# Kernel optimization log

Measured on AMD Instinct MI355X. Metric: run time of the kernel, lower is better.

The kernel has to match this reference:

```python
import jax, jax.numpy as jnp
import numpy as np

B, N, F, H = 2, 2048, 1024, 16
HD = F // H
SQRT_D = float(np.sqrt(F))  # note: module scales by sqrt(in_c), not sqrt(head_dim)


def setup_inputs() -> dict:
    key = jax.random.key(0)
    ks = jax.random.split(key, 9)
    s = 1.0 / np.sqrt(F)
    mk = lambda k: jax.random.uniform(k, (F, F), jnp.float32, -s, s)
    mb = lambda k: jax.random.uniform(k, (F,), jnp.float32, -s, s)
    return {
        "x": jax.random.normal(ks[0], (B, N, F), jnp.float32),
        "Wq": mk(ks[1]), "bq": mb(ks[2]),
        "Wk": mk(ks[3]), "bk": mb(ks[4]),
        "Wv": mk(ks[5]), "bv": mb(ks[6]),
        "Wo": mk(ks[7]), "bo": mb(ks[8]),
    }


def reference(x, Wq, bq, Wk, bk, Wv, bv, Wo, bo):
    b, n, f = x.shape
    # projections (torch Linear: x @ W.T + b); view to (b, n, h, hd)
    q = (x @ Wq.T + bq).reshape(b, n, H, HD)
    k = (x @ Wk.T + bk).reshape(b, n, H, HD)
    v = (x @ Wv.T + bv).reshape(b, n, H, HD)
    score = jnp.einsum('bihd,bjhd->bhij', q, k)
    attn = jax.nn.softmax(score / SQRT_D, axis=-1)
    o = jnp.einsum('bhij,bjhd->bihd', attn, v).reshape(b, n, f)
    return o @ Wo.T + bo
```

## Files before the change

### kernel.cpp

```cpp
#include <hip/hip_runtime.h>
#include <hip/hip_bf16.h>
#include <stdint.h>
#include <stddef.h>

typedef __bf16 bf16;
typedef __attribute__((ext_vector_type(8))) __bf16 bf16x8;
typedef __attribute__((ext_vector_type(4))) __bf16 bf16x4;
typedef __attribute__((ext_vector_type(4))) float f32x4;
typedef __attribute__((ext_vector_type(4))) short s4v;

#define MFMA16(a, b, c) __builtin_amdgcn_mfma_f32_16x16x32_bf16(a, b, c, 0, 0, 0)

__device__ __forceinline__ f32x4 mfma_k16(s4v a, s4v b, f32x4 c) {
#if __has_builtin(__builtin_amdgcn_mfma_f32_16x16x16bf16_1k)
    return __builtin_amdgcn_mfma_f32_16x16x16bf16_1k(a, b, c, 0, 0, 0);
#elif __has_builtin(__builtin_amdgcn_mfma_f32_16x16x16_bf16)
    return __builtin_amdgcn_mfma_f32_16x16x16_bf16(
        __builtin_bit_cast(bf16x4, a), __builtin_bit_cast(bf16x4, b), c, 0, 0, 0);
#else
    asm volatile("v_mfma_f32_16x16x16_bf16 %0, %1, %2, %0\n\ts_nop 7\n\ts_nop 7"
                 : "+v"(c) : "v"(a), "v"(b));
    return c;
#endif
}

#define BB 2
#define SEQ 2048
#define FDIM 1024
#define NH 16
#define HD 64
#define M_TOK 4096
#define N_QKV 3072

#define CSC 0.04508422f

__device__ __forceinline__ void gll16(const bf16* g, bf16* l) {
    __builtin_amdgcn_global_load_lds(
        (const __attribute__((address_space(1))) void*)g,
        (__attribute__((address_space(3))) void*)l, 16, 0, 0);
}

__device__ __forceinline__ bf16 pack_bf16(float f) {
    uint32_t u = __builtin_bit_cast(uint32_t, f);
    uint16_t h = (uint16_t)((u + 0x8000u) >> 16);
    return __builtin_bit_cast(bf16, h);
}

__global__ __launch_bounds__(256) void convert_k(
    const float* __restrict__ x,
    const float* __restrict__ Wq, const float* __restrict__ bq,
    const float* __restrict__ Wk, const float* __restrict__ bk,
    const float* __restrict__ Wv, const float* __restrict__ bv,
    const float* __restrict__ Wo,
    bf16* __restrict__ xb, bf16* __restrict__ Wcat, bf16* __restrict__ Wob,
    float* __restrict__ bcat)
{
    const int tid = blockIdx.x * blockDim.x + threadIdx.x;
    const int nt = gridDim.x * blockDim.x;
    const int NX4 = M_TOK * FDIM / 4;
    const int NW4 = FDIM * FDIM / 4;

    for (int i = tid; i < NX4; i += nt) {
        float4 v = ((const float4*)x)[i];
        bf16x4 o; o[0] = (bf16)v.x; o[1] = (bf16)v.y; o[2] = (bf16)v.z; o[3] = (bf16)v.w;
        ((bf16x4*)xb)[i] = o;
    }
    for (int i = tid; i < NW4; i += nt) {
        float4 v = ((const float4*)Wq)[i];
        bf16x4 o;
        o[0] = (bf16)(v.x * CSC); o[1] = (bf16)(v.y * CSC);
        o[2] = (bf16)(v.z * CSC); o[3] = (bf16)(v.w * CSC);
        ((bf16x4*)Wcat)[i] = o;
        v = ((const float4*)Wk)[i];
        o[0] = (bf16)v.x; o[1] = (bf16)v.y; o[2] = (bf16)v.z; o[3] = (bf16)v.w;
        ((bf16x4*)Wcat)[NW4 + i] = o;
        v = ((const float4*)Wv)[i];
        o[0] = (bf16)v.x; o[1] = (bf16)v.y; o[2] = (bf16)v.z; o[3] = (bf16)v.w;
        ((bf16x4*)Wcat)[2 * NW4 + i] = o;
        v = ((const float4*)Wo)[i];
        o[0] = (bf16)v.x; o[1] = (bf16)v.y; o[2] = (bf16)v.z; o[3] = (bf16)v.w;
        ((bf16x4*)Wob)[i] = o;
    }
    for (int i = tid; i < FDIM; i += nt) {
        bcat[i] = bq[i] * CSC;
        bcat[FDIM + i] = bk[i];
        bcat[2 * FDIM + i] = bv[i];
    }
}

__global__ __launch_bounds__(256) void gemm_bt(
    const bf16* __restrict__ A,
    const bf16* __restrict__ Bw,
    const float* __restrict__ bias,
    bf16* __restrict__ Cb,
    float* __restrict__ Cf,
    bf16* __restrict__ VtOut,
    int M, int N, int K)
{
    __shared__ __align__(16) bf16 As[2][128 * 32];
    __shared__ __align__(16) bf16 Bs[2][128 * 32];

    const int tid = threadIdx.x;
    const int lane = tid & 63;
    const int wave = tid >> 6;
    const int m0 = blockIdx.y * 128;
    const int n0 = blockIdx.x * 128;
    const int wm = (wave >> 1) * 64;
    const int wn = (wave & 1) * 64;
    const int lrow = lane & 15;
    const int lk8 = (lane >> 4) * 8;

    f32x4 acc[4][4] = {};

    const int srow = wave * 16 + (lane >> 2);
    const int scol = (lane & 3) * 8;
    const bf16* Ag = A + (size_t)(m0 + srow) * K + scol;
    const bf16* Bg = Bw + (size_t)(n0 + srow) * K + scol;
    const int wo = (wave * 16) * 32;

    gll16(Ag, &As[0][wo]);
    gll16(Ag + (size_t)64 * K, &As[0][wo + 2048]);
    gll16(Bg, &Bs[0][wo]);
    gll16(Bg + (size_t)64 * K, &Bs[0][wo + 2048]);

    for (int k0 = 0, it = 0; k0 < K; k0 += 32, ++it) {
        const int cur = it & 1;
        __syncthreads();

        if (k0 + 32 < K) {
            const int nxt = cur ^ 1;
            gll16(Ag + k0 + 32, &As[nxt][wo]);
            gll16(Ag + (size_t)64 * K + k0 + 32, &As[nxt][wo + 2048]);
            gll16(Bg + k0 + 32, &Bs[nxt][wo]);
            gll16(Bg + (size_t)64 * K + k0 + 32, &Bs[nxt][wo + 2048]);
        }

        bf16x8 af[4], bfr[4];
#pragma unroll
        for (int s = 0; s < 4; ++s) {
            af[s] = *(const bf16x8*)&As[cur][(wm + s * 16 + lrow) * 32 + lk8];
            bfr[s] = *(const bf16x8*)&Bs[cur][(wn + s * 16 + lrow) * 32 + lk8];
        }
#pragma unroll
        for (int i = 0; i < 4; ++i)
#pragma unroll
            for (int j = 0; j < 4; ++j)
                acc[i][j] = MFMA16(af[i], bfr[j], acc[i][j]);
    }

    const int r0 = (lane >> 4) * 4;
    if (VtOut && n0 >= 2048) {
        const int bql = (m0 >> 11);
#pragma unroll
        for (int i = 0; i < 4; ++i) {
#pragma unroll
            for (int j = 0; j < 4; ++j) {
                const int col = n0 + wn + j * 16 + lrow;
                const float bsv = bias[col];
                const int vh = col - 2048;
                const int row = m0 + wm + i * 16 + r0;
                const int jj = row & (SEQ - 1);
                bf16x4 vv;
#pragma unroll
                for (int r = 0; r < 4; ++r)
                    vv[r] = pack_bf16(acc[i][j][r] + bsv);
                *(bf16x4*)&VtOut[((size_t)bql * 16 * 64 + vh) * SEQ + jj] = vv;
            }
        }
        return;
    }
#pragma unroll
    for (int i = 0; i < 4; ++i) {
#pragma unroll
        for (int j = 0; j < 4; ++j) {
            const int col = n0 + wn + j * 16 + lrow;
            const float bsv = bias[col];
#pragma unroll
            for (int r = 0; r < 4; ++r) {
                const int row = m0 + wm + i * 16 + r0 + r;
                const float v = acc[i][j][r] + bsv;
                if (Cb) Cb[(size_t)row * N + col] = pack_bf16(v);
                else    Cf[(size_t)row * N + col] = v;
            }
        }
    }
}

__global__ __launch_bounds__(256) void attn_k(
    const bf16* __restrict__ QKV,
    const bf16* __restrict__ Vt,
    bf16* __restrict__ O)
{
    const int bh = blockIdx.y;
    const int b = bh >> 4;
    const int h = bh & 15;
    const int lane = threadIdx.x & 63;
    const int wave = threadIdx.x >> 6;
    const int lrow = lane & 15;
    const int quad = lane >> 4;
    const int lk8 = quad * 8;

    __shared__ __align__(16) bf16 Ks[2][2][64 * 32];
    __shared__ __align__(16) bf16 Vs[2][2][64 * 32];

    const size_t base = (size_t)b * SEQ * N_QKV;
    const bf16* Qp = QKV + base + h * HD;
    const bf16* Kp = QKV + base + FDIM + h * HD;
    const bf16* Vtp = Vt + (size_t)bh * HD * SEQ;

    const int qr0 = blockIdx.x * 128 + wave * 32;

    bf16x8 qf[2][2];
#pragma unroll
    for (int qt = 0; qt < 2; ++qt)
#pragma unroll
        for (int ks = 0; ks < 2; ++ks)
            qf[qt][ks] = *(const bf16x8*)(Qp + (size_t)(qr0 + qt * 16 + lrow) * N_QKV
                                          + ks * 32 + lk8);

    bf16x4 ones4;
#pragma unroll
    for (int e = 0; e < 4; ++e) ones4[e] = (bf16)1.0f;
    const s4v onesA = __builtin_bit_cast(s4v, ones4);

    f32x4 o[2][4] = {};
    f32x4 o4[2] = {};

    const int xsw = lrow & 3;
    const int qh = quad >> 1;
    const int ql = (quad & 1) * 4;
    int voff[2][4];
#pragma unroll
    for (int p = 0; p < 2; ++p)
#pragma unroll
        for (int df = 0; df < 4; ++df)
            voff[p][df] = (df * 16 + lrow) * 32 + (((2 * p + qh) ^ xsw) * 8) + ql;

    const int srow = wave * 16 + (lane >> 2);
    const int scol = (lane & 3) * 8;
    const int scolv = (((lane & 3) ^ (srow & 3)) * 8);
    const bf16* kg = Kp + (size_t)srow * N_QKV + scol;
    const bf16* vg = Vtp + (size_t)srow * SEQ + scolv;
    const int wo = (wave * 16) * 32;

    gll16(kg, &Ks[0][0][wo]);
    gll16(kg + 32, &Ks[0][1][wo]);
    gll16(vg, &Vs[0][0][wo]);
    gll16(vg + 32, &Vs[0][1][wo]);
    kg += (size_t)64 * N_QKV;
    vg += 64;

    for (int jt = 0; jt < SEQ / 64; ++jt) {
        const int cur = jt & 1;
        __syncthreads();

        if (jt + 1 < SEQ / 64) {
            gll16(kg, &Ks[cur ^ 1][0][wo]);
            gll16(kg + 32, &Ks[cur ^ 1][1][wo]);
            gll16(vg, &Vs[cur ^ 1][0][wo]);
            gll16(vg + 32, &Vs[cur ^ 1][1][wo]);
            kg += (size_t)64 * N_QKV;
            vg += 64;
        }

        f32x4 Sp[4][2];
#pragma unroll
        for (int jn = 0; jn < 4; ++jn)
#pragma unroll
            for (int qt = 0; qt < 2; ++qt) Sp[jn][qt] = (f32x4){};
#pragma unroll
        for (int ks = 0; ks < 2; ++ks) {
#pragma unroll
            for (int jn = 0; jn < 4; ++jn) {
                bf16x8 kb = *(const bf16x8*)&Ks[cur][ks][(jn * 16 + lrow) * 32 + lk8];
                Sp[jn][0] = MFMA16(kb, qf[0][ks], Sp[jn][0]);
                Sp[jn][1] = MFMA16(kb, qf[1][ks], Sp[jn][1]);
            }
        }

        s4v pB[4][2];
#pragma unroll
        for (int jn = 0; jn < 4; ++jn)
#pragma unroll
            for (int qt = 0; qt < 2; ++qt) {
                bf16x4 t;
#pragma unroll
                for (int r = 0; r < 4; ++r)
                    t[r] = pack_bf16(__builtin_amdgcn_exp2f(Sp[jn][qt][r]));
                pB[jn][qt] = __builtin_bit_cast(s4v, t);
            }

#pragma unroll
        for (int jn = 0; jn < 4; ++jn) {
            const bf16* vbase = &Vs[cur][jn >> 1][0];
            o4[0] = mfma_k16(onesA, pB[jn][0], o4[0]);
            o4[1] = mfma_k16(onesA, pB[jn][1], o4[1]);
#pragma unroll
            for (int df = 0; df < 4; ++df) {
                s4v vA = *(const s4v*)&vbase[voff[jn & 1][df]];
                o[0][df] = mfma_k16(vA, pB[jn][0], o[0][df]);
                o[1][df] = mfma_k16(vA, pB[jn][1], o[1][df]);
            }
        }
    }

#pragma unroll
    for (int qt = 0; qt < 2; ++qt) {
        const float inv = 1.0f / o4[qt][0];
        const int q = qr0 + qt * 16 + lrow;
#pragma unroll
        for (int df = 0; df < 4; ++df) {
            bf16x4 vv;
#pragma unroll
            for (int r = 0; r < 4; ++r)
                vv[r] = pack_bf16(o[qt][df][r] * inv);
            *(bf16x4*)&O[(size_t)(b * SEQ + q) * FDIM + h * HD + df * 16 + quad * 4] = vv;
        }
    }
}

extern "C" void kernel_launch(void* const* d_in, const int* in_sizes, int n_in,
                              void* d_out, int out_size, void* d_ws, size_t ws_size,
                              hipStream_t stream) {
    (void)in_sizes; (void)n_in; (void)out_size; (void)ws_size;
    const float* x  = (const float*)d_in[0];
    const float* Wq = (const float*)d_in[1];
    const float* bq = (const float*)d_in[2];
    const float* Wk = (const float*)d_in[3];
    const float* bk = (const float*)d_in[4];
    const float* Wv = (const float*)d_in[5];
    const float* bv = (const float*)d_in[6];
    const float* Wo = (const float*)d_in[7];
    const float* bo = (const float*)d_in[8];
    float* out = (float*)d_out;

    char* ws = (char*)d_ws;
    bf16* xb    = (bf16*)(ws);
    bf16* Wcat  = (bf16*)(ws + 8388608);
    bf16* Wob   = (bf16*)(ws + 14680064);
    float* bcat = (float*)(ws + 16777216);
    bf16* QKV   = (bf16*)(ws + 16789504);
    bf16* Vt    = (bf16*)(ws + 41955328);
    bf16* Ob    = xb;

    convert_k<<<dim3(1024), dim3(256), 0, stream>>>(x, Wq, bq, Wk, bk, Wv, bv, Wo,
                                                    xb, Wcat, Wob, bcat);
    gemm_bt<<<dim3(N_QKV / 128, M_TOK / 128), dim3(256), 0, stream>>>(
        xb, Wcat, bcat, QKV, nullptr, Vt, M_TOK, N_QKV, FDIM);
    attn_k<<<dim3(SEQ / 128, BB * NH), dim3(256), 0, stream>>>(QKV, Vt, Ob);
    gemm_bt<<<dim3(FDIM / 128, M_TOK / 128), dim3(256), 0, stream>>>(
        Ob, Wob, bo, nullptr, out, nullptr, M_TOK, FDIM, FDIM);
}
```

Before: 215.4 us.

## Use K=32 MFMA for PV by permuting Vt layout to match score fragments

Changes the P·V and row-sum accumulation from 16x16x16 MFMAs to 16x16x32 MFMAs by packing two score tiles into one 8-element bf16 operand. The V projection epilogue now writes Vt with a permuted sequence index within each 64-block, so that V fragments line up with the packed P layout. This drops the XOR swizzle on V loads. It also adds a packed bf16 conversion helper and reorganises the QK loop to start from a zero accumulator. The aim is to halve the MFMA instruction count for PV and cut conversion overhead, at the cost of possible LDS bank conflicts now that the V swizzle is gone.

```diff
diff --git a/kernel.cpp b/kernel.cpp
--- a/kernel.cpp
+++ b/kernel.cpp
@@ -6,23 +6,10 @@
 typedef __bf16 bf16;
 typedef __attribute__((ext_vector_type(8))) __bf16 bf16x8;
 typedef __attribute__((ext_vector_type(4))) __bf16 bf16x4;
+typedef __attribute__((ext_vector_type(2))) __bf16 bf16x2;
 typedef __attribute__((ext_vector_type(4))) float f32x4;
-typedef __attribute__((ext_vector_type(4))) short s4v;
 
 #define MFMA16(a, b, c) __builtin_amdgcn_mfma_f32_16x16x32_bf16(a, b, c, 0, 0, 0)
-
-__device__ __forceinline__ f32x4 mfma_k16(s4v a, s4v b, f32x4 c) {
-#if __has_builtin(__builtin_amdgcn_mfma_f32_16x16x16bf16_1k)
-    return __builtin_amdgcn_mfma_f32_16x16x16bf16_1k(a, b, c, 0, 0, 0);
-#elif __has_builtin(__builtin_amdgcn_mfma_f32_16x16x16_bf16)
-    return __builtin_amdgcn_mfma_f32_16x16x16_bf16(
-        __builtin_bit_cast(bf16x4, a), __builtin_bit_cast(bf16x4, b), c, 0, 0, 0);
-#else
-    asm volatile("v_mfma_f32_16x16x16_bf16 %0, %1, %2, %0\n\ts_nop 7\n\ts_nop 7"
-                 : "+v"(c) : "v"(a), "v"(b));
-    return c;
-#endif
-}
 
 #define BB 2
 #define SEQ 2048
@@ -44,6 +31,17 @@
     uint32_t u = __builtin_bit_cast(uint32_t, f);
     uint16_t h = (uint16_t)((u + 0x8000u) >> 16);
     return __builtin_bit_cast(bf16, h);
+}
+
+__device__ __forceinline__ uint32_t pk2(float a, float b) {
+#if __has_builtin(__builtin_amdgcn_cvt_pk_bf16_f32)
+    bf16x2 t = __builtin_amdgcn_cvt_pk_bf16_f32(a, b);
+    return __builtin_bit_cast(uint32_t, t);
+#else
+    uint32_t ua = __builtin_bit_cast(uint32_t, a) + 0x8000u;
+    uint32_t ub = __builtin_bit_cast(uint32_t, b) + 0x8000u;
+    return __builtin_amdgcn_perm(ub, ua, 0x07060302);
+#endif
 }
 
 __global__ __launch_bounds__(256) void convert_k(
@@ -160,11 +158,14 @@
                 const int vh = col - 2048;
                 const int row = m0 + wm + i * 16 + r0;
                 const int jj = row & (SEQ - 1);
+                const int g = jj & 63;
+                const int jj2 = (jj & ~63) | ((g >> 5) << 5)
+                              | (((g >> 2) & 3) << 3) | (((g >> 4) & 1) << 2);
                 bf16x4 vv;
 #pragma unroll
                 for (int r = 0; r < 4; ++r)
                     vv[r] = pack_bf16(acc[i][j][r] + bsv);
-                *(bf16x4*)&VtOut[((size_t)bql * 16 * 64 + vh) * SEQ + jj] = vv;
+                *(bf16x4*)&VtOut[((size_t)bql * 16 * 64 + vh) * SEQ + jj2] = vv;
             }
         }
         return;
@@ -218,29 +219,19 @@
             qf[qt][ks] = *(const bf16x8*)(Qp + (size_t)(qr0 + qt * 16 + lrow) * N_QKV
                                           + ks * 32 + lk8);
 
-    bf16x4 ones4;
-#pragma unroll
-    for (int e = 0; e < 4; ++e) ones4[e] = (bf16)1.0f;
-    const s4v onesA = __builtin_bit_cast(s4v, ones4);
+    bf16x8 ones8;
+#pragma unroll
+    for (int e = 0; e < 8; ++e) ones8[e] = (bf16)1.0f;
+
+    const f32x4 zf = {0.f, 0.f, 0.f, 0.f};
 
     f32x4 o[2][4] = {};
     f32x4 o4[2] = {};
 
-    const int xsw = lrow & 3;
-    const int qh = quad >> 1;
-    const int ql = (quad & 1) * 4;
-    int voff[2][4];
-#pragma unroll
-    for (int p = 0; p < 2; ++p)
-#pragma unroll
-        for (int df = 0; df < 4; ++df)
-            voff[p][df] = (df * 16 + lrow) * 32 + (((2 * p + qh) ^ xsw) * 8) + ql;
-
     const int srow = wave * 16 + (lane >> 2);
     const int scol = (lane & 3) * 8;
-    const int scolv = (((lane & 3) ^ (srow & 3)) * 8);
     const bf16* kg = Kp + (size_t)srow * N_QKV + scol;
-    const bf16* vg = Vtp + (size_t)srow * SEQ + scolv;
+    const bf16* vg = Vtp + (size_t)srow * SEQ + scol;
     const int wo = (wave * 16) * 32;
 
     gll16(kg, &Ks[0][0][wo]);
@@ -265,41 +256,39 @@
 
         f32x4 Sp[4][2];
 #pragma unroll
-        for (int jn = 0; jn < 4; ++jn)
-#pragma unroll
-            for (int qt = 0; qt < 2; ++qt) Sp[jn][qt] = (f32x4){};
-#pragma unroll
-        for (int ks = 0; ks < 2; ++ks) {
-#pragma unroll
-            for (int jn = 0; jn < 4; ++jn) {
-                bf16x8 kb = *(const bf16x8*)&Ks[cur][ks][(jn * 16 + lrow) * 32 + lk8];
-                Sp[jn][0] = MFMA16(kb, qf[0][ks], Sp[jn][0]);
-                Sp[jn][1] = MFMA16(kb, qf[1][ks], Sp[jn][1]);
+        for (int jn = 0; jn < 4; ++jn) {
+            bf16x8 kb0 = *(const bf16x8*)&Ks[cur][0][(jn * 16 + lrow) * 32 + lk8];
+            bf16x8 kb1 = *(const bf16x8*)&Ks[cur][1][(jn * 16 + lrow) * 32 + lk8];
+            Sp[jn][0] = MFMA16(kb0, qf[0][0], zf);
+            Sp[jn][0] = MFMA16(kb1, qf[0][1], Sp[jn][0]);
+            Sp[jn][1] = MFMA16(kb0, qf[1][0], zf);
+            Sp[jn][1] = MFMA16(kb1, qf[1][1], Sp[jn][1]);
+        }
+
+#pragma unroll
+        for (int p = 0; p < 2; ++p) {
+            union { bf16x8 v; uint32_t d[4]; } pb[2];
+#pragma unroll
+            for (int qt = 0; qt < 2; ++qt) {
+                const f32x4 s0 = Sp[2 * p][qt];
+                const f32x4 s1 = Sp[2 * p + 1][qt];
+                pb[qt].d[0] = pk2(__builtin_amdgcn_exp2f(s0[0]),
+                                  __builtin_amdgcn_exp2f(s0[1]));
+                pb[qt].d[1] = pk2(__builtin_amdgcn_exp2f(s0[2]),
+                                  __builtin_amdgcn_exp2f(s0[3]));
+                pb[qt].d[2] = pk2(__builtin_amdgcn_exp2f(s1[0]),
+                                  __builtin_amdgcn_exp2f(s1[1]));
+                pb[qt].d[3] = pk2(__builtin_amdgcn_exp2f(s1[2]),
+                                  __builtin_amdgcn_exp2f(s1[3]));
             }
-        }
-
-        s4v pB[4][2];
-#pragma unroll
-        for (int jn = 0; jn < 4; ++jn)
-#pragma unroll
-            for (int qt = 0; qt < 2; ++qt) {
-                bf16x4 t;
-#pragma unroll
-                for (int r = 0; r < 4; ++r)
-                    t[r] = pack_bf16(__builtin_amdgcn_exp2f(Sp[jn][qt][r]));
-                pB[jn][qt] = __builtin_bit_cast(s4v, t);
-            }
-
-#pragma unroll
-        for (int jn = 0; jn < 4; ++jn) {
-            const bf16* vbase = &Vs[cur][jn >> 1][0];
-            o4[0] = mfma_k16(onesA, pB[jn][0], o4[0]);
-            o4[1] = mfma_k16(onesA, pB[jn][1], o4[1]);
+
+            o4[0] = MFMA16(ones8, pb[0].v, o4[0]);
+            o4[1] = MFMA16(ones8, pb[1].v, o4[1]);
 #pragma unroll
             for (int df = 0; df < 4; ++df) {
-                s4v vA = *(const s4v*)&vbase[voff[jn & 1][df]];
-                o[0][df] = mfma_k16(vA, pB[jn][0], o[0][df]);
-                o[1][df] = mfma_k16(vA, pB[jn][1], o[1][df]);
+                bf16x8 vA = *(const bf16x8*)&Vs[cur][p][(df * 16 + lrow) * 32 + lk8];
+                o[0][df] = MFMA16(vA, pb[0].v, o[0][df]);
+                o[1][df] = MFMA16(vA, pb[1].v, o[1][df]);
             }
         }
     }
```

New measurement: 204.6 us. -5.0%, faster.
